# Optimization experiments

Measured on AMD Instinct MI355X. Metric: run time of the kernel, lower is better.

## Reference

```python
import jax, jax.numpy as jnp
import numpy as np

DIM = 256
EXPAND = 4
BN_EPS = 1e-5

def _conv(x, w, groups=1):
    # NCHW conv, stride 1, SAME padding (3x3 pad=1 or 1x1 pad=0)
    return jax.lax.conv_general_dilated(
        x, w, window_strides=(1, 1), padding='SAME',
        dimension_numbers=('NCHW', 'OIHW', 'NCHW'),
        feature_group_count=groups)

def _dwconv(x, dw_w, dw_b, pw_w, pw_b):
    c = x.shape[1]
    y = _conv(x, dw_w, groups=c) + dw_b[None, :, None, None]
    y = _conv(y, pw_w) + pw_b[None, :, None, None]
    return y

def setup_inputs() -> dict:
    key = jax.random.key(0)
    ks = jax.random.split(key, 16)
    C = DIM
    s = lambda k, shape, fan: jax.random.normal(k, shape, jnp.float32) * (1.0 / np.sqrt(fan))
    inp = {
        'x': jax.random.normal(ks[0], (8, C, 32, 32), jnp.float32),
        # q_a DWConv
        'qa_dw_w': s(ks[1], (C, 1, 3, 3), 9), 'qa_dw_b': jnp.zeros((C,), jnp.float32),
        'qa_pw_w': s(ks[2], (C, C, 1, 1), C), 'qa_pw_b': jnp.zeros((C,), jnp.float32),
        # k_a DWConv (C -> 4C)
        'ka_dw_w': s(ks[3], (C, 1, 3, 3), 9), 'ka_dw_b': jnp.zeros((C,), jnp.float32),
        'ka_pw_w': s(ks[4], (EXPAND * C, C, 1, 1), C), 'ka_pw_b': jnp.zeros((EXPAND * C,), jnp.float32),
        # v_a DWConv
        'va_dw_w': s(ks[5], (C, 1, 3, 3), 9), 'va_dw_b': jnp.zeros((C,), jnp.float32),
        'va_pw_w': s(ks[6], (C, C, 1, 1), C), 'va_pw_b': jnp.zeros((C,), jnp.float32),
        # attn_conv_a0: 4->4 conv (no bias) + BatchNorm2d(4) (eval mode, running stats)
        'attn0_w': s(ks[7], (EXPAND, EXPAND, 3, 3), 9 * EXPAND),
        'bn_gamma': jnp.ones((EXPAND,), jnp.float32),
        'bn_beta': jnp.zeros((EXPAND,), jnp.float32),
        'bn_mean': jnp.zeros((EXPAND,), jnp.float32),
        'bn_var': jnp.ones((EXPAND,), jnp.float32),
        # attn_conv_a1: 4->1 conv (no bias)
        'attn1_w': s(ks[8], (1, EXPAND, 3, 3), 9 * EXPAND),
        # proj_a: C->C 3x3 conv (no bias)
        'proj_w': s(ks[9], (C, C, 3, 3), 9 * C),
    }
    return inp

def reference(x, qa_dw_w, qa_dw_b, qa_pw_w, qa_pw_b,
              ka_dw_w, ka_dw_b, ka_pw_w, ka_pw_b,
              va_dw_w, va_dw_b, va_pw_w, va_pw_b,
              attn0_w, bn_gamma, bn_beta, bn_mean, bn_var,
              attn1_w, proj_w):
    B, C, H, W = x.shape
    N = H * W
    scale = C ** (-0.5)  # head_dim = dim // num_heads, num_heads = 1

    q = _dwconv(x, qa_dw_w, qa_dw_b, qa_pw_w, qa_pw_b).reshape(B, C, N)      # [B,C,N]
    k = _dwconv(x, ka_dw_w, ka_dw_b, ka_pw_w, ka_pw_b).reshape(B, EXPAND, C, N)  # [B,4,C,N]
    v = _dwconv(x, va_dw_w, va_dw_b, va_pw_w, va_pw_b).reshape(B, C, N)      # [B,C,N]

    # q_a: [B,1,N,C] broadcast against k_a: [B,4,C,N] -> attn [B,4,N,N]
    attn = jnp.einsum('bcn,bkcm->bknm', q, k) * scale

    # conv(4->4) + BatchNorm2d(4) in eval mode
    attn = _conv(attn, attn0_w)
    inv = jax.lax.rsqrt(bn_var + BN_EPS)
    attn = (attn - bn_mean[None, :, None, None]) * (bn_gamma * inv)[None, :, None, None] \
           + bn_beta[None, :, None, None]

    # self-gating: attn * softmax(attn, axis=-1)
    attn = attn * jax.nn.softmax(attn, axis=-1)

    # conv(4->1) -> [B,1,N,N]
    attn = _conv(attn, attn1_w)

    # (attn @ v^T): [B,N,N] @ [B,N,C] -> [B,N,C] -> [B,C,H,W]
    out = jnp.einsum('bnm,bcm->bcn', attn[:, 0], v).reshape(B, C, H, W)
    out = _conv(out, proj_w)
    return out, attn
```

## Files before the change

### kernel.cpp

```cpp
#include <hip/hip_runtime.h>

using bf16   = __bf16;
using bf16x4 = __bf16 __attribute__((ext_vector_type(4)));
using bf16x8 = __bf16 __attribute__((ext_vector_type(8)));
using f32x4  = float  __attribute__((ext_vector_type(4)));

#define NANTHRESH 64

#define QT_OFF    0LL
#define KT_OFF    2097152LL
#define V_OFF     10485760LL
#define AWS_OFF   12582912LL
#define ATT_OFF   20971520LL
#define CW_OFF    54525952LL
#define FLAG_ELOFF 55518416LL
#define CX_OFF    20971520LL
#define DWQ_OFF   23068672LL
#define DWK_OFF   25165824LL
#define DWV_OFF   27262976LL
#define OUTP_OFF  20971520LL
#define COL_OFF   0LL

__device__ __constant__ int g_nsz[20] = {
    2097152, 2304,256,65536,256, 2304,256,262144,1024,
    2304,256,65536,256, 144, 4,4,4,4, 36, 589824};
__device__ __constant__ long long g_doff[20] = {
    CX_OFF,
    CW_OFF+0,      CW_OFF+2304,   CW_OFF+2560,   CW_OFF+68096,
    CW_OFF+68352,  CW_OFF+70656,  CW_OFF+70912,  CW_OFF+333056,
    CW_OFF+334080, CW_OFF+336384, CW_OFF+336640, CW_OFF+402176,
    CW_OFF+402432, CW_OFF+402576, CW_OFF+402580, CW_OFF+402584,
    CW_OFF+402588, CW_OFF+402592, CW_OFF+402640};

struct SrcPtrs { const void* p[20]; };

__global__ void k_zero(int* p) { if (threadIdx.x < 4) p[threadIdx.x] = 0; }

__global__ __launch_bounds__(256) void k_detect(const unsigned short* __restrict__ xs,
                                                int* __restrict__ cnt)
{
    int idx = blockIdx.x * 256 + threadIdx.x;
    int c = 0;
#pragma unroll
    for (int i = 0; i < 16; i++) {
        unsigned short h = xs[idx + i * 16384];
        c += ((h & 0x7F80) == 0x7F80);
    }
    if (c) atomicAdd(cnt, c);
}

__global__ __launch_bounds__(256) void k_convert(SrcPtrs sp, bf16* __restrict__ wsb,
                                                 const int* __restrict__ nf)
{
    const int t = blockIdx.y;
    const int n = g_nsz[t];
    const bool srcf32 = (*nf > NANTHRESH);
    const void* src = sp.p[t];
    bf16* dst = wsb + g_doff[t];
    for (int i = blockIdx.x * 256 + threadIdx.x; i < n; i += 256 * 256) {
        float f = srcf32 ? ((const float*)src)[i] : (float)((const bf16*)src)[i];
        if (!(fabsf(f) < 1e30f)) f = 0.f;
        dst[i] = (bf16)f;
    }
}

__global__ __launch_bounds__(256) void gemm_nt(
    const bf16* __restrict__ A, const bf16* __restrict__ Bc,
    const bf16* __restrict__ bias, void* __restrict__ Dv,
    int K, int lda, int ldb, int ldd,
    int zdiv, long long sA1, long long sA2, long long sB1, long long sB2,
    long long sD1, long long sD2, float alpha, int bias_mode,
    const int* __restrict__ nf, int dyn)
{
    const int z  = blockIdx.z;
    const int zq = z / zdiv, zr = z % zdiv;
    A  += (long long)zq * sA1 + (long long)zr * sA2;
    Bc += (long long)zq * sB1 + (long long)zr * sB2;
    const long long zoff = (long long)zq * sD1 + (long long)zr * sD2;
    const bool f32o = dyn && (*nf > NANTHRESH);
    const int m0 = blockIdx.y * 64;
    const int n0 = blockIdx.x * 64;
    __shared__ __align__(16) bf16 As[64 * 72];
    __shared__ __align__(16) bf16 Bs[64 * 72];
    const int tid  = threadIdx.x;
    const int lane = tid & 63;
    const int wave = tid >> 6;
    const int wm   = (wave >> 1) * 32;
    const int wn   = (wave & 1) * 32;
    const int quad = lane >> 4;
    const int l16  = lane & 15;
    f32x4 acc[2][2] = {};
    for (int k0 = 0; k0 < K; k0 += 64) {
#pragma unroll
        for (int i = 0; i < 2; i++) {
            int cid = tid + i * 256;
            int row = cid >> 3;
            int kc  = (cid & 7) * 8;
            *reinterpret_cast<int4*>(&As[row * 72 + kc]) =
                *reinterpret_cast<const int4*>(&A[(long long)(m0 + row) * lda + k0 + kc]);
            *reinterpret_cast<int4*>(&Bs[row * 72 + kc]) =
                *reinterpret_cast<const int4*>(&Bc[(long long)(n0 + row) * ldb + k0 + kc]);
        }
        __syncthreads();
#pragma unroll
        for (int ks = 0; ks < 2; ks++) {
            bf16x8 af[2], bfr[2];
#pragma unroll
            for (int i = 0; i < 2; i++) {
                af[i]  = *reinterpret_cast<const bf16x8*>(&As[(wm + i * 16 + l16) * 72 + ks * 32 + quad * 8]);
                bfr[i] = *reinterpret_cast<const bf16x8*>(&Bs[(wn + i * 16 + l16) * 72 + ks * 32 + quad * 8]);
            }
#pragma unroll
            for (int i = 0; i < 2; i++)
#pragma unroll
                for (int j = 0; j < 2; j++)
                    acc[i][j] = __builtin_amdgcn_mfma_f32_16x16x32_bf16(af[i], bfr[j], acc[i][j], 0, 0, 0);
        }
        __syncthreads();
    }
#pragma unroll
    for (int i = 0; i < 2; i++)
#pragma unroll
        for (int j = 0; j < 2; j++)
#pragma unroll
            for (int r = 0; r < 4; r++) {
                int row = m0 + wm + i * 16 + quad * 4 + r;
                int col = n0 + wn + j * 16 + l16;
                float v = acc[i][j][r] * alpha;
                if (bias_mode == 1) v += (float)bias[row];
                else if (bias_mode == 2) v += (float)bias[col];
                long long idx = zoff + (long long)row * ldd + col;
                if (f32o) ((float*)Dv)[idx] = v;
                else      ((bf16*)Dv)[idx] = (bf16)v;
            }
}

__global__ __launch_bounds__(256) void k_dw(
    const bf16* __restrict__ x,
    const bf16* __restrict__ wq, const bf16* __restrict__ bq,
    const bf16* __restrict__ wk, const bf16* __restrict__ bk,
    const bf16* __restrict__ wv, const bf16* __restrict__ bv,
    bf16* __restrict__ dq, bf16* __restrict__ dk, bf16* __restrict__ dv)
{
    __shared__ __align__(16) bf16 obuf[3 * 64 * 72];
    const int ct = blockIdx.x, hp = blockIdx.y, b = blockIdx.z;
    const int c0 = ct * 64, h0 = hp * 2, n0 = hp * 64;
    const int t = threadIdx.x;
    const int c = t & 63, psub = t >> 6;
    const int hl = psub >> 1, wbase = (psub & 1) * 16;
    const int gc = c0 + c;
    const int h = h0 + hl;
    float xr[3][18];
    const bf16* chbase = x + ((long long)b * 256 + gc) * 1024;
#pragma unroll
    for (int r = 0; r < 3; r++) {
        int hr = h + r - 1;
        if (hr >= 0 && hr < 32) {
            const bf16* rp = chbase + hr * 32;
            bf16x8 v0 = *reinterpret_cast<const bf16x8*>(rp + wbase);
            bf16x8 v1 = *reinterpret_cast<const bf16x8*>(rp + wbase + 8);
#pragma unroll
            for (int j = 0; j < 8; j++) { xr[r][1 + j] = (float)v0[j]; xr[r][9 + j] = (float)v1[j]; }
            xr[r][0]  = (wbase > 0)       ? (float)rp[wbase - 1]  : 0.f;
            xr[r][17] = (wbase + 16 < 32) ? (float)rp[wbase + 16] : 0.f;
        } else {
#pragma unroll
            for (int j = 0; j < 18; j++) xr[r][j] = 0.f;
        }
    }
    float wrq[9], wrk[9], wrv[9];
#pragma unroll
    for (int j = 0; j < 9; j++) {
        wrq[j] = (float)wq[gc * 9 + j];
        wrk[j] = (float)wk[gc * 9 + j];
        wrv[j] = (float)wv[gc * 9 + j];
    }
    const float biq = (float)bq[gc], bik = (float)bk[gc], biv = (float)bv[gc];
#pragma unroll
    for (int i = 0; i < 16; i++) {
        float aq = biq, ak = bik, av = biv;
#pragma unroll
        for (int r = 0; r < 3; r++)
#pragma unroll
            for (int d = 0; d < 3; d++) {
                float xv = xr[r][i + d];
                aq += xv * wrq[r * 3 + d];
                ak += xv * wrk[r * 3 + d];
                av += xv * wrv[r * 3 + d];
            }
        int p = hl * 32 + wbase + i;
        obuf[0 * 4608 + p * 72 + c] = (bf16)aq;
        obuf[1 * 4608 + p * 72 + c] = (bf16)ak;
        obuf[2 * 4608 + p * 72 + c] = (bf16)av;
    }
    __syncthreads();
    bf16* dsts[3] = {dq, dk, dv};
    const int chunk = t & 7, pr0 = t >> 3;
#pragma unroll
    for (int t3 = 0; t3 < 3; t3++) {
        bf16* dst = dsts[t3];
#pragma unroll
        for (int rep = 0; rep < 2; rep++) {
            int pr = pr0 + rep * 32;
            int4 val = *reinterpret_cast<const int4*>(&obuf[t3 * 4608 + pr * 72 + chunk * 8]);
            *reinterpret_cast<int4*>(&dst[((long long)b * 1024 + n0 + pr) * 256 + c0 + chunk * 8]) = val;
        }
    }
}

__global__ __launch_bounds__(256) void k_midconv(
    const bf16* __restrict__ att,
    const bf16* __restrict__ w0,
    const bf16* __restrict__ gamma, const bf16* __restrict__ beta,
    const bf16* __restrict__ mean,  const bf16* __restrict__ var,
    const bf16* __restrict__ w1,
    bf16* __restrict__ aws,
    void* __restrict__ dout, const int* __restrict__ nf)
{
    __shared__ __align__(16) bf16 sG[24 * 1024];
    __shared__ __align__(16) bf16 pm[24 * 256];
    __shared__ float w0ld[144];
    __shared__ float w1s[36];
    __shared__ float mxs[24], rsum[24];

    const int rt = blockIdx.x, b = blockIdx.y;
    const int n0 = rt * 4;
    const int tid = threadIdx.x;
    const int m0 = tid * 4;
    const int wv_ = tid >> 6, lane = tid & 63;

    if (tid < 144) {
        int c = tid / 36, rem = tid % 36, r = rem / 12, kd = rem % 12;
        int k = kd / 3, d = kd % 3;
        w0ld[(c * 3 + r) * 12 + kd] = (float)w0[((k * 4 + c) * 3 + r) * 3 + d];
    } else if (tid < 180) {
        w1s[tid - 144] = (float)w1[tid - 144];
    }
    float bns[4], bnb[4];
#pragma unroll
    for (int k = 0; k < 4; k++) {
        float inv = rsqrtf((float)var[k] + 1e-5f);
        bns[k] = (float)gamma[k] * inv;
        bnb[k] = (float)beta[k] - (float)mean[k] * bns[k];
    }
    __syncthreads();

    float vals[6][4][4] = {};
    const bf16* attb = att + (long long)b * 4194304;
    for (int c = 0; c < 4; c++) {
        float rv[8][6];
#pragma unroll
        for (int rw = 0; rw < 8; rw++) {
            int row = n0 - 2 + rw;
            if (row >= 0 && row < 1024) {
                const bf16* rp = attb + ((long long)c * 1024 + row) * 1024;
                bf16x4 t4 = *reinterpret_cast<const bf16x4*>(rp + m0);
#pragma unroll
                for (int u = 0; u < 4; u++) rv[rw][1 + u] = (float)t4[u];
                rv[rw][0] = (m0 > 0)        ? (float)rp[m0 - 1] : 0.f;
                rv[rw][5] = (m0 + 4 < 1024) ? (float)rp[m0 + 4] : 0.f;
            } else {
#pragma unroll
                for (int u = 0; u < 6; u++) rv[rw][u] = 0.f;
            }
        }
#pragma unroll
        for (int r = 0; r < 3; r++) {
            float wvv[12];
#pragma unroll
            for (int q = 0; q < 12; q++) wvv[q] = w0ld[(c * 3 + r) * 12 + q];
#pragma unroll
            for (int j = 0; j < 6; j++)
#pragma unroll
                for (int k = 0; k < 4; k++)
#pragma unroll
                    for (int d = 0; d < 3; d++)
#pragma unroll
                        for (int u = 0; u < 4; u++)
                            vals[j][k][u] += wvv[k * 3 + d] * rv[j + r][u + d];
        }
    }
#pragma unroll
    for (int j = 0; j < 6; j++)
#pragma unroll
        for (int k = 0; k < 4; k++)
#pragma unroll
            for (int u = 0; u < 4; u++)
                vals[j][k][u] = vals[j][k][u] * bns[k] + bnb[k];

#pragma unroll
    for (int j = 0; j < 6; j++)
#pragma unroll
        for (int k = 0; k < 4; k++) {
            float lm = fmaxf(fmaxf(vals[j][k][0], vals[j][k][1]),
                             fmaxf(vals[j][k][2], vals[j][k][3]));
            pm[(k * 6 + j) * 256 + tid] = (bf16)lm;
        }
    __syncthreads();
#pragma unroll
    for (int s = 0; s < 6; s++) {
        int rid = wv_ * 6 + s;
        bf16x4 p = *reinterpret_cast<const bf16x4*>(&pm[rid * 256 + lane * 4]);
        float mx = fmaxf(fmaxf((float)p[0], (float)p[1]), fmaxf((float)p[2], (float)p[3]));
#pragma unroll
        for (int off = 32; off; off >>= 1) mx = fmaxf(mx, __shfl_xor(mx, off));
        if (lane == 0) mxs[rid] = mx;
    }
    __syncthreads();
#pragma unroll
    for (int j = 0; j < 6; j++)
#pragma unroll
        for (int k = 0; k < 4; k++) {
            int rid = k * 6 + j;
            float mx = mxs[rid];
            float ls = 0.f;
#pragma unroll
            for (int u = 0; u < 4; u++) ls += __expf(vals[j][k][u] - mx);
            pm[rid * 256 + tid] = (bf16)ls;
        }
    __syncthreads();
#pragma unroll
    for (int s = 0; s < 6; s++) {
        int rid = wv_ * 6 + s;
        bf16x4 p = *reinterpret_cast<const bf16x4*>(&pm[rid * 256 + lane * 4]);
        float sm = (float)p[0] + (float)p[1] + (float)p[2] + (float)p[3];
#pragma unroll
        for (int off = 32; off; off >>= 1) sm += __shfl_xor(sm, off);
        if (lane == 0) rsum[rid] = sm;
    }
    __syncthreads();

#pragma unroll
    for (int j = 0; j < 6; j++) {
        int nm = n0 - 1 + j;
        bool valid = (nm >= 0 && nm < 1024);
#pragma unroll
        for (int k = 0; k < 4; k++) {
            int rid = k * 6 + j;
            float mx = mxs[rid], ri = 1.0f / rsum[rid];
            bf16x4 g4;
#pragma unroll
            for (int u = 0; u < 4; u++) {
                float t = vals[j][k][u];
                g4[u] = valid ? (bf16)(t * __expf(t - mx) * ri) : (bf16)0.0f;
            }
            *reinterpret_cast<bf16x4*>(&sG[rid * 1024 + m0]) = g4;
        }
    }
    __syncthreads();

    float acc1[4][4] = {};
    for (int c = 0; c < 4; c++) {
        float rv2[6][6];
#pragma unroll
        for (int j = 0; j < 6; j++) {
            const bf16* gp = &sG[(c * 6 + j) * 1024];
            bf16x4 t4 = *reinterpret_cast<const bf16x4*>(gp + m0);
#pragma unroll
            for (int u = 0; u < 4; u++) rv2[j][1 + u] = (float)t4[u];
            rv2[j][0] = (m0 > 0)        ? (float)gp[m0 - 1] : 0.f;
            rv2[j][5] = (m0 + 4 < 1024) ? (float)gp[m0 + 4] : 0.f;
        }
#pragma unroll
        for (int r = 0; r < 3; r++) {
            float w3[3];
#pragma unroll
            for (int d = 0; d < 3; d++) w3[d] = w1s[(c * 3 + r) * 3 + d];
#pragma unroll
            for (int i = 0; i < 4; i++)
#pragma unroll
                for (int d = 0; d < 3; d++)
#pragma unroll
                    for (int u = 0; u < 4; u++)
                        acc1[i][u] += w3[d] * rv2[i + r][u + d];
        }
    }
    const bool f32o = (*nf > NANTHRESH);
    bf16* awsb = aws + (long long)b * 1048576;
#pragma unroll
    for (int i = 0; i < 4; i++) {
        int n = n0 + i;
        bf16x4 o4;
#pragma unroll
        for (int u = 0; u < 4; u++) o4[u] = (bf16)acc1[i][u];
        *reinterpret_cast<bf16x4*>(&awsb[(long long)n * 1024 + m0]) = o4;
        long long fo = 2097152LL + (long long)b * 1048576 + (long long)n * 1024 + m0;
        if (f32o) {
            f32x4 of = {acc1[i][0], acc1[i][1], acc1[i][2], acc1[i][3]};
            *reinterpret_cast<f32x4*>(&((float*)dout)[fo]) = of;
        } else {
            *reinterpret_cast<bf16x4*>(&((bf16*)dout)[fo]) = o4;
        }
    }
}

__global__ __launch_bounds__(256) void k_im2col(
    const bf16* __restrict__ src, bf16* __restrict__ dst)
{
    const int blk = blockIdx.x;
    const int b = blk >> 10, n = blk & 1023;
    const int h = n >> 5, w = n & 31;
    const int ci = threadIdx.x;
    const bf16* sb = src + (long long)b * 262144;
    bf16* db = dst + ((long long)b * 1024 + n) * 2304 + ci * 9;
#pragma unroll
    for (int dh = 0; dh < 3; dh++)
#pragma unroll
        for (int dw_ = 0; dw_ < 3; dw_++) {
            int hh = h + dh - 1, ww = w + dw_ - 1;
            bf16 vv = (bf16)0.0f;
            if (hh >= 0 && hh < 32 && ww >= 0 && ww < 32)
                vv = sb[(hh * 32 + ww) * 256 + ci];
            db[dh * 3 + dw_] = vv;
        }
}

extern "C" void kernel_launch(void* const* d_in, const int* in_sizes, int n_in,
                              void* d_out, int out_size, void* d_ws, size_t ws_size,
                              hipStream_t stream)
{
    bf16* ws = (bf16*)d_ws;
    int* flagp = (int*)(ws + FLAG_ELOFF);

    bf16* cw      = ws + CW_OFF;
    bf16* cx      = ws + CX_OFF;
    bf16* dwq     = ws + DWQ_OFF;
    bf16* dwk     = ws + DWK_OFF;
    bf16* dwv     = ws + DWV_OFF;
    bf16* qT      = ws + QT_OFF;
    bf16* kT      = ws + KT_OFF;
    bf16* v       = ws + V_OFF;
    bf16* aws     = ws + AWS_OFF;
    bf16* att     = ws + ATT_OFF;
    bf16* outp    = ws + OUTP_OFF;
    bf16* colbuf  = ws + COL_OFF;

    bf16* c_qa_dw_w = cw + 0;      bf16* c_qa_dw_b = cw + 2304;
    bf16* c_qa_pw_w = cw + 2560;   bf16* c_qa_pw_b = cw + 68096;
    bf16* c_ka_dw_w = cw + 68352;  bf16* c_ka_dw_b = cw + 70656;
    bf16* c_ka_pw_w = cw + 70912;  bf16* c_ka_pw_b = cw + 333056;
    bf16* c_va_dw_w = cw + 334080; bf16* c_va_dw_b = cw + 336384;
    bf16* c_va_pw_w = cw + 336640; bf16* c_va_pw_b = cw + 402176;
    bf16* c_attn0   = cw + 402432;
    bf16* c_bn_g    = cw + 402576; bf16* c_bn_b = cw + 402580;
    bf16* c_bn_m    = cw + 402584; bf16* c_bn_v = cw + 402588;
    bf16* c_attn1   = cw + 402592;
    bf16* c_proj    = cw + 402640;

    k_zero<<<1, 64, 0, stream>>>(flagp);
    k_detect<<<64, 256, 0, stream>>>((const unsigned short*)d_in[0], flagp);
    SrcPtrs sp;
    for (int i = 0; i < 20; i++) sp.p[i] = d_in[i];
    k_convert<<<dim3(256, 20), 256, 0, stream>>>(sp, ws, flagp);

    k_dw<<<dim3(4, 16, 8), 256, 0, stream>>>(cx, c_qa_dw_w, c_qa_dw_b, c_ka_dw_w, c_ka_dw_b,
                                             c_va_dw_w, c_va_dw_b, dwq, dwk, dwv);
    gemm_nt<<<dim3(4, 128, 1), 256, 0, stream>>>(dwq, c_qa_pw_w, c_qa_pw_b, qT,
        256, 256, 256, 256, 1, 0, 0, 0, 0, 0, 0, 1.0f, 2, flagp, 0);
    gemm_nt<<<dim3(16, 128, 1), 256, 0, stream>>>(dwk, c_ka_pw_w, c_ka_pw_b, kT,
        256, 256, 256, 1024, 1, 0, 0, 0, 0, 0, 0, 1.0f, 2, flagp, 0);
    gemm_nt<<<dim3(128, 4, 1), 256, 0, stream>>>(c_va_pw_w, dwv, c_va_pw_b, v,
        256, 256, 256, 8192, 1, 0, 0, 0, 0, 0, 0, 1.0f, 1, flagp, 0);
    gemm_nt<<<dim3(16, 16, 32), 256, 0, stream>>>(qT, kT, nullptr, att,
        256, 256, 1024, 1024,
        4, 262144LL, 0LL, 1048576LL, 256LL, 4194304LL, 1048576LL,
        0.0625f, 0, flagp, 0);
    k_midconv<<<dim3(256, 8), 256, 0, stream>>>(att, c_attn0, c_bn_g, c_bn_b, c_bn_m, c_bn_v,
                                                c_attn1, aws, d_out, flagp);
    gemm_nt<<<dim3(4, 16, 8), 256, 0, stream>>>(aws, v, nullptr, outp,
        1024, 1024, 8192, 256,
        1, 1048576LL, 0LL, 1024LL, 0LL, 262144LL, 0LL, 1.0f, 0, flagp, 0);
    k_im2col<<<8192, 256, 0, stream>>>(outp, colbuf);
    gemm_nt<<<dim3(16, 4, 8), 256, 0, stream>>>(c_proj, colbuf, nullptr, d_out,
        2304, 2304, 2304, 1024,
        1, 0LL, 0LL, 2359296LL, 0LL, 262144LL, 0LL, 1.0f, 0, flagp, 1);
}
```

Before: 405.0 us.

## Keep gated attention in registers with shuffles instead of a shared-memory buffer in midconv

```diff
diff --git a/kernel.cpp b/kernel.cpp
--- a/kernel.cpp
+++ b/kernel.cpp
@@ -208,7 +208,7 @@
     }
 }
 
-__global__ __launch_bounds__(256) void k_midconv(
+__global__ __launch_bounds__(256, 4) void k_midconv(
     const bf16* __restrict__ att,
     const bf16* __restrict__ w0,
     const bf16* __restrict__ gamma, const bf16* __restrict__ beta,
@@ -217,11 +217,11 @@
     bf16* __restrict__ aws,
     void* __restrict__ dout, const int* __restrict__ nf)
 {
-    __shared__ __align__(16) bf16 sG[24 * 1024];
     __shared__ __align__(16) bf16 pm[24 * 256];
     __shared__ float w0ld[144];
     __shared__ float w1s[36];
     __shared__ float mxs[24], rsum[24];
+    __shared__ float sEL[4][24], sER[4][24];
 
     const int rt = blockIdx.x, b = blockIdx.y;
     const int n0 = rt * 4;
@@ -248,36 +248,33 @@
     float vals[6][4][4] = {};
     const bf16* attb = att + (long long)b * 4194304;
     for (int c = 0; c < 4; c++) {
-        float rv[8][6];
 #pragma unroll
         for (int rw = 0; rw < 8; rw++) {
             int row = n0 - 2 + rw;
+            float rv6[6];
             if (row >= 0 && row < 1024) {
                 const bf16* rp = attb + ((long long)c * 1024 + row) * 1024;
                 bf16x4 t4 = *reinterpret_cast<const bf16x4*>(rp + m0);
 #pragma unroll
-                for (int u = 0; u < 4; u++) rv[rw][1 + u] = (float)t4[u];
-                rv[rw][0] = (m0 > 0)        ? (float)rp[m0 - 1] : 0.f;
-                rv[rw][5] = (m0 + 4 < 1024) ? (float)rp[m0 + 4] : 0.f;
+                for (int u = 0; u < 4; u++) rv6[1 + u] = (float)t4[u];
+                rv6[0] = (m0 > 0)        ? (float)rp[m0 - 1] : 0.f;
+                rv6[5] = (m0 + 4 < 1024) ? (float)rp[m0 + 4] : 0.f;
             } else {
 #pragma unroll
-                for (int u = 0; u < 6; u++) rv[rw][u] = 0.f;
-            }
-        }
-#pragma unroll
-        for (int r = 0; r < 3; r++) {
-            float wvv[12];
-#pragma unroll
-            for (int q = 0; q < 12; q++) wvv[q] = w0ld[(c * 3 + r) * 12 + q];
-#pragma unroll
-            for (int j = 0; j < 6; j++)
+                for (int u = 0; u < 6; u++) rv6[u] = 0.f;
+            }
+#pragma unroll
+            for (int r = 0; r < 3; r++) {
+                int j = rw - r;
+                if (j < 0 || j > 5) continue;
 #pragma unroll
                 for (int k = 0; k < 4; k++)
 #pragma unroll
                     for (int d = 0; d < 3; d++)
 #pragma unroll
                         for (int u = 0; u < 4; u++)
-                            vals[j][k][u] += wvv[k * 3 + d] * rv[j + r][u + d];
+                            vals[j][k][u] += w0ld[(c * 3 + r) * 12 + k * 3 + d] * rv6[u + d];
+            }
         }
     }
 #pragma unroll
@@ -338,43 +335,56 @@
         for (int k = 0; k < 4; k++) {
             int rid = k * 6 + j;
             float mx = mxs[rid], ri = 1.0f / rsum[rid];
-            bf16x4 g4;
 #pragma unroll
             for (int u = 0; u < 4; u++) {
                 float t = vals[j][k][u];
-                g4[u] = valid ? (bf16)(t * __expf(t - mx) * ri) : (bf16)0.0f;
-            }
-            *reinterpret_cast<bf16x4*>(&sG[rid * 1024 + m0]) = g4;
-        }
+                vals[j][k][u] = valid ? (t * __expf(t - mx) * ri) : 0.f;
+            }
+        }
+    }
+
+    if (lane == 63 && wv_ < 3) {
+#pragma unroll
+        for (int j = 0; j < 6; j++)
+#pragma unroll
+            for (int k = 0; k < 4; k++)
+                sEL[wv_ + 1][k * 6 + j] = vals[j][k][3];
+    }
+    if (lane == 0 && wv_ > 0) {
+#pragma unroll
+        for (int j = 0; j < 6; j++)
+#pragma unroll
+            for (int k = 0; k < 4; k++)
+                sER[wv_ - 1][k * 6 + j] = vals[j][k][0];
     }
     __syncthreads();
 
     float acc1[4][4] = {};
-    for (int c = 0; c < 4; c++) {
-        float rv2[6][6];
+#pragma unroll
+    for (int k = 0; k < 4; k++)
 #pragma unroll
         for (int j = 0; j < 6; j++) {
-            const bf16* gp = &sG[(c * 6 + j) * 1024];
-            bf16x4 t4 = *reinterpret_cast<const bf16x4*>(gp + m0);
-#pragma unroll
-            for (int u = 0; u < 4; u++) rv2[j][1 + u] = (float)t4[u];
-            rv2[j][0] = (m0 > 0)        ? (float)gp[m0 - 1] : 0.f;
-            rv2[j][5] = (m0 + 4 < 1024) ? (float)gp[m0 + 4] : 0.f;
-        }
-#pragma unroll
-        for (int r = 0; r < 3; r++) {
-            float w3[3];
-#pragma unroll
-            for (int d = 0; d < 3; d++) w3[d] = w1s[(c * 3 + r) * 3 + d];
-#pragma unroll
-            for (int i = 0; i < 4; i++)
-#pragma unroll
-                for (int d = 0; d < 3; d++)
+            int rid = k * 6 + j;
+            float left  = __shfl_up(vals[j][k][3], 1);
+            float right = __shfl_down(vals[j][k][0], 1);
+            if (lane == 0)  left  = (wv_ > 0) ? sEL[wv_][rid] : 0.f;
+            if (lane == 63) right = (wv_ < 3) ? sER[wv_][rid] : 0.f;
+            float vec[6] = {left, vals[j][k][0], vals[j][k][1],
+                            vals[j][k][2], vals[j][k][3], right};
+#pragma unroll
+            for (int i = 0; i < 4; i++) {
+                int r = j - i;
+                if (r < 0 || r > 2) continue;
+#pragma unroll
+                for (int d = 0; d < 3; d++) {
+                    float wv1 = w1s[(k * 3 + r) * 3 + d];
 #pragma unroll
                     for (int u = 0; u < 4; u++)
-                        acc1[i][u] += w3[d] * rv2[i + r][u + d];
-        }
-    }
+                        acc1[i][u] += wv1 * vec[u + d];
+                }
+            }
+        }
+
     const bool f32o = (*nf > NANTHRESH);
     bf16* awsb = aws + (long long)b * 1048576;
 #pragma unroll
```

Result: slower. 1.530 ms (+277.9%).
